# Performance work log

Hardware: AMD Instinct MI355X
Metric: run time of the kernel (lower is better)

The kernel has to match this reference:

```python
import jax, jax.numpy as jnp
import numpy as np

B, S, D, H = 2, 2048, 1024, 16
HD = D // H  # 64


def setup_inputs() -> dict:
    key = jax.random.key(0)
    ks = jax.random.split(key, 5)
    sc = 1.0 / np.sqrt(D)
    return {
        "x": jax.random.normal(ks[0], (B, S, D), jnp.float32),
        "wq": jax.random.normal(ks[1], (D, D), jnp.float32) * sc,
        "bq": jnp.zeros((D,), jnp.float32),
        "wk": jax.random.normal(ks[2], (D, D), jnp.float32) * sc,
        "bk": jnp.zeros((D,), jnp.float32),
        "wv": jax.random.normal(ks[3], (D, D), jnp.float32) * sc,
        "bv": jnp.zeros((D,), jnp.float32),
        "wo": jax.random.normal(ks[4], (D, D), jnp.float32) * sc,
        "bo": jnp.zeros((D,), jnp.float32),
    }


def _rope_tables(seq_len, dim):
    inv_freq = 1.0 / (10000.0 ** (jnp.arange(0, dim, 2, dtype=jnp.float32) / dim))
    t = jnp.arange(seq_len, dtype=jnp.float32)
    freqs = jnp.einsum("i,j->ij", t, inv_freq)  # [S, dim/2]
    emb = jnp.concatenate([freqs, freqs], axis=-1)  # [S, dim]
    return jnp.cos(emb)[None, None], jnp.sin(emb)[None, None]  # [1,1,S,dim]


def _rotate_half(x):
    x1, x2 = x[..., : x.shape[-1] // 2], x[..., x.shape[-1] // 2 :]
    return jnp.concatenate([-x2, x1], axis=-1)


def reference(x, wq, bq, wk, bk, wv, bv, wo, bo):
    b, s, d = x.shape
    h, hd = H, d // H
    # projections (torch Linear: x @ W.T + b) -> [b, h, s, hd]
    def proj(w, bias):
        return (x @ w.T + bias).reshape(b, s, h, hd).transpose(0, 2, 1, 3)

    q, k, v = proj(wq, bq), proj(wk, bk), proj(wv, bv)
    cos, sin = _rope_tables(s, hd)
    q = q * cos + _rotate_half(q) * sin
    k = k * cos + _rotate_half(k) * sin
    scores = jnp.einsum("bhqd,bhkd->bhqk", q, k) / jnp.sqrt(jnp.float32(hd))
    attn = jax.nn.softmax(scores, axis=-1)
    out = jnp.einsum("bhqk,bhkd->bhqd", attn, v)
    out = out.transpose(0, 2, 1, 3).reshape(b, s, d)
    return out @ wo.T + bo
```

## Files before the change

kernel.cpp:

```cpp
#include <hip/hip_runtime.h>
#include <hip/hip_bf16.h>

#define Bq 2
#define Sq 2048
#define Dq 1024
#define Hq 16
#define QSCALE 0.18033688011112042f

typedef __attribute__((ext_vector_type(8))) short short8;
typedef __attribute__((ext_vector_type(4))) float floatx4;
typedef unsigned short ushort_t;

#define VMCNT0() asm volatile("s_waitcnt vmcnt(0)" ::: "memory")
#define GLDS(src, dst) __builtin_amdgcn_global_load_lds( \
    (const __attribute__((address_space(1))) void*)(src), \
    (__attribute__((address_space(3))) void*)(dst), 16, 0, 0)

__device__ __forceinline__ ushort_t f2bf(float f) {
    union { float f; unsigned u; } v; v.f = f;
    unsigned u = v.u;
    u += 0x7fffu + ((u >> 16) & 1u);
    return (ushort_t)(u >> 16);
}

__device__ __forceinline__ unsigned pk_bf16(float a, float b) {
    union { __hip_bfloat162 h; unsigned u; } c;
    c.h = __float22bfloat162_rn(float2{a, b});
    return c.u;
}

__device__ __forceinline__ void cvt8(const float* __restrict__ in, ushort_t* __restrict__ out, int i) {
    const float4* p = (const float4*)in + (size_t)i * 2;
    float4 a = p[0], b = p[1];
    ushort4 lo, hi;
    lo.x = f2bf(a.x); lo.y = f2bf(a.y); lo.z = f2bf(a.z); lo.w = f2bf(a.w);
    hi.x = f2bf(b.x); hi.y = f2bf(b.y); hi.z = f2bf(b.z); hi.w = f2bf(b.w);
    *(ushort4*)(out + (size_t)i * 8)     = lo;
    *(ushort4*)(out + (size_t)i * 8 + 4) = hi;
}

__global__ void prep(const float* __restrict__ x,
                     const float* __restrict__ wq, const float* __restrict__ wk,
                     const float* __restrict__ wv, const float* __restrict__ wo,
                     ushort_t* __restrict__ xb,
                     ushort_t* __restrict__ wqb, ushort_t* __restrict__ wkb,
                     ushort_t* __restrict__ wvb, ushort_t* __restrict__ wob,
                     float* __restrict__ cost, float* __restrict__ sint) {
    int b = blockIdx.x;
    if (b < 2048) {
        cvt8(x, xb, b * 256 + threadIdx.x);
    } else if (b < 4096) {
        int w = (b - 2048) >> 9;
        int i = ((b - 2048) & 511) * 256 + threadIdx.x;
        const float* src = (w == 0) ? wq : (w == 1) ? wk : (w == 2) ? wv : wo;
        ushort_t* dst    = (w == 0) ? wqb : (w == 1) ? wkb : (w == 2) ? wvb : wob;
        cvt8(src, dst, i);
    } else {
        int i = (b - 4096) * 256 + threadIdx.x;
        int s = i >> 5, f = i & 31;
        float invf = powf(10000.0f, -(float)f / 32.0f);
        float ang = (float)s * invf;
        cost[i] = cosf(ang);
        sint[i] = sinf(ang);
    }
}

__global__ __launch_bounds__(256, 3) void gemm_qkv(
    const ushort_t* __restrict__ xb,
    const ushort_t* __restrict__ wqb, const ushort_t* __restrict__ wkb, const ushort_t* __restrict__ wvb,
    const float* __restrict__ bq, const float* __restrict__ bk, const float* __restrict__ bv,
    const float* __restrict__ cost, const float* __restrict__ sint,
    ushort_t* __restrict__ qout, ushort_t* __restrict__ kout, ushort_t* __restrict__ vtout)
{
    __shared__ ushort_t As0[128 * 32], As1[128 * 32];
    __shared__ ushort_t Bs0[128 * 32], Bs1[128 * 32];
    const int mode = blockIdx.z;
    const ushort_t* W  = (mode == 0) ? wqb : (mode == 1) ? wkb : wvb;
    const float* bias  = (mode == 0) ? bq  : (mode == 1) ? bk  : bv;

    const int t = threadIdx.x;
    const int lane = t & 63;
    const int wid = t >> 6;
    const int l15 = lane & 15, lk = lane >> 4;
    const int wr = wid >> 1, wc = wid & 1;
    const int rowBase = blockIdx.y * 128;
    const int colBase = blockIdx.x * 128;

    floatx4 acc[4][4] = {};

    const char* aSrc[2];
    const char* bSrc[2];
    int ldso[2];
#pragma unroll
    for (int issue = 0; issue < 2; ++issue) {
        int ldsoff = issue * 4096 + t * 16;
        int row = ldsoff >> 6;
        int cb  = ldsoff & 63;
        ldso[issue] = ldsoff;
        aSrc[issue] = (const char*)xb + (size_t)(rowBase + row) * 2048 + cb;
        bSrc[issue] = (const char*)W  + (size_t)(colBase + row) * 2048 + cb;
    }

    auto STAGE = [&](ushort_t* Ad, ushort_t* Bd) {
#pragma unroll
        for (int issue = 0; issue < 2; ++issue) {
            GLDS(aSrc[issue], (char*)Ad + ldso[issue]);
            GLDS(bSrc[issue], (char*)Bd + ldso[issue]);
        }
        aSrc[0] += 64; aSrc[1] += 64; bSrc[0] += 64; bSrc[1] += 64;
    };

    auto KSTEP = [&](const ushort_t* Ac, const ushort_t* Bc, int knext, ushort_t* An, ushort_t* Bn) {
        if (knext < Dq) STAGE(An, Bn);
        short8 a[4], b[4];
#pragma unroll
        for (int m = 0; m < 4; ++m)
            a[m] = *(const short8*)((const char*)Ac + (wr * 64 + m * 16 + l15) * 64 + lk * 16);
#pragma unroll
        for (int n = 0; n < 4; ++n)
            b[n] = *(const short8*)((const char*)Bc + (wc * 64 + n * 16 + l15) * 64 + lk * 16);
        __builtin_amdgcn_s_setprio(1);
#pragma unroll
        for (int m = 0; m < 4; ++m)
#pragma unroll
            for (int n = 0; n < 4; ++n)
                acc[m][n] = __builtin_amdgcn_mfma_f32_16x16x32_bf16(a[m], b[n], acc[m][n], 0, 0, 0);
        __builtin_amdgcn_s_setprio(0);
        VMCNT0();
        __syncthreads();
    };

    STAGE(As0, Bs0);
    VMCNT0();
    __syncthreads();

#pragma unroll 1
    for (int k0 = 0; k0 < Dq; k0 += 64) {
        KSTEP(As0, Bs0, k0 + 32, As1, Bs1);
        KSTEP(As1, Bs1, k0 + 64, As0, Bs0);
    }

    const int colW = colBase + wc * 64;
    const int hh = colW >> 6;

    if (mode < 2) {
        ushort_t* outp = (mode == 0) ? qout : kout;
        const float osc = (mode == 0) ? QSCALE : 1.0f;
#pragma unroll
        for (int m = 0; m < 4; ++m) {
            int rg0 = rowBase + wr * 64 + m * 16 + lk * 4;
#pragma unroll
            for (int n2 = 0; n2 < 2; ++n2) {
                int d0 = n2 * 16 + l15;
                float b0 = bias[colW + d0];
                float b2 = bias[colW + d0 + 32];
#pragma unroll
                for (int r = 0; r < 4; ++r) {
                    int rg = rg0 + r;
                    int bb = rg >> 11;
                    int s  = rg & 2047;
                    float c  = cost[s * 32 + d0];
                    float sn = sint[s * 32 + d0];
                    float a0 = acc[m][n2][r]     + b0;
                    float a2 = acc[m][n2 + 2][r] + b2;
                    float o0 = (a0 * c - a2 * sn) * osc;
                    float o2 = (a2 * c + a0 * sn) * osc;
                    size_t base = ((size_t)(bb * Hq + hh) * Sq + s) * 64;
                    outp[base + d0]      = f2bf(o0);
                    outp[base + d0 + 32] = f2bf(o2);
                }
            }
        }
    } else {
#pragma unroll
        for (int m = 0; m < 4; ++m) {
            int rg0 = rowBase + wr * 64 + m * 16 + lk * 4;
            int bb  = rg0 >> 11;
            int s0  = rg0 & 2047;
            int g   = (s0 & 63) >> 2;
            int ng  = (g >> 3) * 8 + (g & 3) * 2 + ((g >> 2) & 1);
            int s2b = (s0 & ~63) + ng * 4;
#pragma unroll
            for (int n = 0; n < 4; ++n) {
                int d = n * 16 + l15;
                float bb_ = bias[colW + d];
#pragma unroll
                for (int r = 0; r < 4; ++r)
                    vtout[((size_t)(bb * Hq + hh) * 64 + d) * Sq + s2b + r] = f2bf(acc[m][n][r] + bb_);
            }
        }
    }
}

__global__ __launch_bounds__(256, 3) void flash_attn(
    const ushort_t* __restrict__ qbuf, const ushort_t* __restrict__ kbuf,
    const ushort_t* __restrict__ vtbuf, ushort_t* __restrict__ abuf)
{
    __shared__ char Ks0[16384], Ks1[16384];
    __shared__ char Vs0[16384], Vs1[16384];

    const int t = threadIdx.x, lane = t & 63, wid = t >> 6;
    const int l15 = lane & 15, lk = lane >> 4;

    int flat = blockIdx.y * 16 + blockIdx.x;
    flat = (flat & 7) * 64 + (flat >> 3);
    const int qtile = flat & 15, bh = flat >> 4;
    const int bpos = bh >> 4, h = bh & 15;
    const int qbase = qtile * 128 + wid * 32;

    const ushort_t* Qp = qbuf + ((size_t)bh * Sq + qbase) * 64;
    short8 qf[2][2];
#pragma unroll
    for (int mq = 0; mq < 2; ++mq)
#pragma unroll
        for (int kk = 0; kk < 2; ++kk)
            qf[mq][kk] = *(const short8*)(Qp + (mq * 16 + l15) * 64 + kk * 32 + lk * 8);

    short8 onesf;
#pragma unroll
    for (int j = 0; j < 8; ++j) onesf[j] = (short)0x3F80;

    floatx4 oacc[2][4] = {};
    floatx4 lacc[2] = {};

    int off_[4][2];
#pragma unroll
    for (int n = 0; n < 4; ++n) {
        int swz = (l15 & 7) << 4;
#pragma unroll
        for (int kk = 0; kk < 2; ++kk)
            off_[n][kk] = (n * 16 + l15) * 128 + ((kk * 64 + lk * 16) ^ swz);
    }

    const char* Kg = (const char*)kbuf  + (size_t)bh * Sq * 128;
    const char* Vg = (const char*)vtbuf + (size_t)bh * 64 * Sq * 2;
    unsigned kOff[2], vOff[2];
    int ldso[2];
#pragma unroll
    for (int issue = 0; issue < 2; ++issue) {
        int ldsoff = issue * 4096 + t * 16;
        int row = ldsoff >> 7;
        int pb  = ldsoff & 127;
        int lb  = pb ^ ((row & 7) << 4);
        ldso[issue] = ldsoff;
        kOff[issue] = (unsigned)(row * 128 + lb);
        vOff[issue] = (unsigned)(row * 4096 + lb);
    }

    auto STAGE = [&](char* Kd, char* Vd) {
#pragma unroll
        for (int issue = 0; issue < 2; ++issue) {
            GLDS(Kg + kOff[issue],        Kd + ldso[issue]);
            GLDS(Kg + kOff[issue] + 8192, Kd + 8192 + ldso[issue]);
            GLDS(Vg + vOff[issue],        Vd + ldso[issue]);
            GLDS(Vg + vOff[issue] + 128,  Vd + 8192 + ldso[issue]);
        }
        kOff[0] += 16384; kOff[1] += 16384; vOff[0] += 256; vOff[1] += 256;
    };

    auto TILE = [&](const char* Kc, const char* Vc, bool doStage, char* Kn, char* Vn) {
        if (doStage) STAGE(Kn, Vn);

#pragma unroll
        for (int sub = 0; sub < 2; ++sub) {
            const char* Kcs = Kc + sub * 8192;
            const char* Vcs = Vc + sub * 8192;

            short8 kf[4][2];
#pragma unroll
            for (int n = 0; n < 4; ++n)
#pragma unroll
                for (int kk = 0; kk < 2; ++kk)
                    kf[n][kk] = *(const short8*)(Kcs + off_[n][kk]);

            floatx4 sacc[2][4] = {};
            __builtin_amdgcn_s_setprio(1);
#pragma unroll
            for (int kk = 0; kk < 2; ++kk)
#pragma unroll
                for (int n = 0; n < 4; ++n)
#pragma unroll
                    for (int mq = 0; mq < 2; ++mq)
                        sacc[mq][n] = __builtin_amdgcn_mfma_f32_16x16x32_bf16(kf[n][kk], qf[mq][kk], sacc[mq][n], 0, 0, 0);
            __builtin_amdgcn_s_setprio(0);

            short8 vf[4][2];
#pragma unroll
            for (int n = 0; n < 4; ++n)
#pragma unroll
                for (int kb = 0; kb < 2; ++kb)
                    vf[n][kb] = *(const short8*)(Vcs + off_[n][kb]);

            short8 paf[2][2];
#pragma unroll
            for (int mq = 0; mq < 2; ++mq) {
                float p[4][4];
#pragma unroll
                for (int n = 0; n < 4; ++n)
#pragma unroll
                    for (int r = 0; r < 4; ++r)
                        p[n][r] = __builtin_exp2f(sacc[mq][n][r]);
#pragma unroll
                for (int kb = 0; kb < 2; ++kb) {
                    union { unsigned u[4]; short8 v; } pu;
                    pu.u[0] = pk_bf16(p[2 * kb][0],     p[2 * kb][1]);
                    pu.u[1] = pk_bf16(p[2 * kb][2],     p[2 * kb][3]);
                    pu.u[2] = pk_bf16(p[2 * kb + 1][0], p[2 * kb + 1][1]);
                    pu.u[3] = pk_bf16(p[2 * kb + 1][2], p[2 * kb + 1][3]);
                    paf[mq][kb] = pu.v;
                }
            }

            __builtin_amdgcn_s_setprio(1);
#pragma unroll
            for (int kb = 0; kb < 2; ++kb) {
#pragma unroll
                for (int n = 0; n < 4; ++n)
#pragma unroll
                    for (int mq = 0; mq < 2; ++mq)
                        oacc[mq][n] = __builtin_amdgcn_mfma_f32_16x16x32_bf16(paf[mq][kb], vf[n][kb], oacc[mq][n], 0, 0, 0);
#pragma unroll
                for (int mq = 0; mq < 2; ++mq)
                    lacc[mq] = __builtin_amdgcn_mfma_f32_16x16x32_bf16(paf[mq][kb], onesf, lacc[mq], 0, 0, 0);
            }
            __builtin_amdgcn_s_setprio(0);
        }

        VMCNT0();
        __syncthreads();
    };

    STAGE(Ks0, Vs0);
    VMCNT0();
    __syncthreads();

#pragma unroll 1
    for (int i = 0; i < 7; ++i) {
        TILE(Ks0, Vs0, true, Ks1, Vs1);
        TILE(Ks1, Vs1, true, Ks0, Vs0);
    }
    TILE(Ks0, Vs0, true,  Ks1, Vs1);
    TILE(Ks1, Vs1, false, Ks0, Vs0);

#pragma unroll
    for (int mq = 0; mq < 2; ++mq)
#pragma unroll
        for (int r = 0; r < 4; ++r) {
            float linv = 1.0f / lacc[mq][r];
            int srow = qbase + mq * 16 + lk * 4 + r;
            size_t base = ((size_t)bpos * Sq + srow) * Dq + h * 64;
#pragma unroll
            for (int n = 0; n < 4; ++n)
                abuf[base + n * 16 + l15] = f2bf(oacc[mq][n][r] * linv);
        }
}

__global__ __launch_bounds__(256, 3) void gemm_out(
    const ushort_t* __restrict__ ab, const ushort_t* __restrict__ wob,
    const float* __restrict__ bo, float* __restrict__ out)
{
    __shared__ ushort_t As0[128 * 64], As1[128 * 64];
    __shared__ ushort_t Bs0[64 * 64],  Bs1[64 * 64];
    const int t = threadIdx.x;
    const int lane = t & 63;
    const int wid = t >> 6;
    const int l15 = lane & 15, lk = lane >> 4;
    const int wr = wid >> 1, wc = wid & 1;
    const int rowBase = blockIdx.y * 128;
    const int colBase = blockIdx.x * 64;

    floatx4 acc[4][2] = {};

    const int swz = (l15 & 7) << 4;
    int aoff_[4][2], boff_[2][2];
#pragma unroll
    for (int m = 0; m < 4; ++m)
#pragma unroll
        for (int kk = 0; kk < 2; ++kk)
            aoff_[m][kk] = (wr * 64 + m * 16 + l15) * 128 + ((kk * 64 + lk * 16) ^ swz);
#pragma unroll
    for (int n = 0; n < 2; ++n)
#pragma unroll
        for (int kk = 0; kk < 2; ++kk)
            boff_[n][kk] = (wc * 32 + n * 16 + l15) * 128 + ((kk * 64 + lk * 16) ^ swz);

    const char* aSrc[4];
    const char* bSrc[2];
    int ldsoA[4], ldsoB[2];
#pragma unroll
    for (int issue = 0; issue < 4; ++issue) {
        int ldsoff = issue * 4096 + t * 16;
        int row = ldsoff >> 7;
        int pb  = ldsoff & 127;
        int lb  = pb ^ ((row & 7) << 4);
        ldsoA[issue] = ldsoff;
        aSrc[issue] = (const char*)ab + (size_t)(rowBase + row) * 2048 + lb;
    }
#pragma unroll
    for (int issue = 0; issue < 2; ++issue) {
        int ldsoff = issue * 4096 + t * 16;
        int row = ldsoff >> 7;
        int pb  = ldsoff & 127;
        int lb  = pb ^ ((row & 7) << 4);
        ldsoB[issue] = ldsoff;
        bSrc[issue] = (const char*)wob + (size_t)(colBase + row) * 2048 + lb;
    }

    auto STAGE = [&](ushort_t* Ad, ushort_t* Bd) {
#pragma unroll
        for (int issue = 0; issue < 4; ++issue)
            GLDS(aSrc[issue], (char*)Ad + ldsoA[issue]);
#pragma unroll
        for (int issue = 0; issue < 2; ++issue)
            GLDS(bSrc[issue], (char*)Bd + ldsoB[issue]);
#pragma unroll
        for (int issue = 0; issue < 4; ++issue) aSrc[issue] += 128;
        bSrc[0] += 128; bSrc[1] += 128;
    };

    auto KSTEP = [&](const ushort_t* Ac, const ushort_t* Bc, int knext, ushort_t* An, ushort_t* Bn) {
        if (knext < Dq) STAGE(An, Bn);
        short8 a[4][2], b[2][2];
#pragma unroll
        for (int m = 0; m < 4; ++m)
#pragma unroll
            for (int kk = 0; kk < 2; ++kk)
                a[m][kk] = *(const short8*)((const char*)Ac + aoff_[m][kk]);
#pragma unroll
        for (int n = 0; n < 2; ++n)
#pragma unroll
            for (int kk = 0; kk < 2; ++kk)
                b[n][kk] = *(const short8*)((const char*)Bc + boff_[n][kk]);
        __builtin_amdgcn_s_setprio(1);
#pragma unroll
        for (int kk = 0; kk < 2; ++kk)
#pragma unroll
            for (int m = 0; m < 4; ++m)
#pragma unroll
                for (int n = 0; n < 2; ++n)
                    acc[m][n] = __builtin_amdgcn_mfma_f32_16x16x32_bf16(a[m][kk], b[n][kk], acc[m][n], 0, 0, 0);
        __builtin_amdgcn_s_setprio(0);
        VMCNT0();
        __syncthreads();
    };

    STAGE(As0, Bs0);
    VMCNT0();
    __syncthreads();

#pragma unroll 1
    for (int k0 = 0; k0 < Dq; k0 += 128) {
        KSTEP(As0, Bs0, k0 + 64,  As1, Bs1);
        KSTEP(As1, Bs1, k0 + 128, As0, Bs0);
    }

    const int colW = colBase + wc * 32;
#pragma unroll
    for (int m = 0; m < 4; ++m) {
        int rg0 = rowBase + wr * 64 + m * 16 + lk * 4;
#pragma unroll
        for (int n = 0; n < 2; ++n) {
            int colg = colW + n * 16 + l15;
            float bb_ = bo[colg];
#pragma unroll
            for (int r = 0; r < 4; ++r)
                out[(size_t)(rg0 + r) * Dq + colg] = acc[m][n][r] + bb_;
        }
    }
}

extern "C" void kernel_launch(void* const* d_in, const int* in_sizes, int n_in,
                              void* d_out, int out_size, void* d_ws, size_t ws_size,
                              hipStream_t stream) {
    (void)in_sizes; (void)n_in; (void)out_size;
    const float* x  = (const float*)d_in[0];
    const float* wq = (const float*)d_in[1];
    const float* bq = (const float*)d_in[2];
    const float* wk = (const float*)d_in[3];
    const float* bk = (const float*)d_in[4];
    const float* wv = (const float*)d_in[5];
    const float* bv = (const float*)d_in[6];
    const float* wo = (const float*)d_in[7];
    const float* bo = (const float*)d_in[8];
    float* out = (float*)d_out;

    if (ws_size < 50855936) return;
    char* ws = (char*)d_ws;
    ushort_t* xb   = (ushort_t*)(ws + 0);
    ushort_t* wqb  = (ushort_t*)(ws + 8388608);
    ushort_t* wkb  = (ushort_t*)(ws + 10485760);
    ushort_t* wvb  = (ushort_t*)(ws + 12582912);
    ushort_t* wob  = (ushort_t*)(ws + 14680064);
    ushort_t* qb   = (ushort_t*)(ws + 16777216);
    ushort_t* kb   = (ushort_t*)(ws + 25165824);
    ushort_t* vtb  = (ushort_t*)(ws + 33554432);
    ushort_t* abuf = (ushort_t*)(ws + 41943040);
    float*    cost = (float*)(ws + 50331648);
    float*    sint = (float*)(ws + 50593792);

    prep<<<4352, 256, 0, stream>>>(x, wq, wk, wv, wo, xb, wqb, wkb, wvb, wob, cost, sint);
    gemm_qkv<<<dim3(8, 32, 3), 256, 0, stream>>>(xb, wqb, wkb, wvb, bq, bk, bv, cost, sint, qb, kb, vtb);
    flash_attn<<<dim3(16, 32), 256, 0, stream>>>(qb, kb, vtb, abuf);
    gemm_out<<<dim3(16, 32), 256, 0, stream>>>(abuf, wob, bo, out);
}
```

Before: 119.4 us.

## Double QKV GEMM K-tile with swizzled LDS and halve attention KV tile

The QKV projection GEMM now stages 64-wide K slices (128-byte rows) instead of 32-wide ones. It uses an XOR swizzle on both the global source offsets and the LDS reads to avoid bank conflicts, and runs two MFMA k-substeps per barrier, halving the number of syncs. Launch bounds drop to 2 blocks per CU to fit the larger LDS footprint. Separately, the flash attention kernel shrinks its K/V tile from 128 to 64 keys per stage, doubling the loop count. This halves its LDS use, presumably for occupancy, at the cost of more barriers.

```diff
diff --git a/kernel.cpp b/kernel.cpp
--- a/kernel.cpp
+++ b/kernel.cpp
@@ -65,15 +65,15 @@
     }
 }
 
-__global__ __launch_bounds__(256, 3) void gemm_qkv(
+__global__ __launch_bounds__(256, 2) void gemm_qkv(
     const ushort_t* __restrict__ xb,
     const ushort_t* __restrict__ wqb, const ushort_t* __restrict__ wkb, const ushort_t* __restrict__ wvb,
     const float* __restrict__ bq, const float* __restrict__ bk, const float* __restrict__ bv,
     const float* __restrict__ cost, const float* __restrict__ sint,
     ushort_t* __restrict__ qout, ushort_t* __restrict__ kout, ushort_t* __restrict__ vtout)
 {
-    __shared__ ushort_t As0[128 * 32], As1[128 * 32];
-    __shared__ ushort_t Bs0[128 * 32], Bs1[128 * 32];
+    __shared__ ushort_t As0[128 * 64], As1[128 * 64];
+    __shared__ ushort_t Bs0[128 * 64], Bs1[128 * 64];
     const int mode = blockIdx.z;
     const ushort_t* W  = (mode == 0) ? wqb : (mode == 1) ? wkb : wvb;
     const float* bias  = (mode == 0) ? bq  : (mode == 1) ? bk  : bv;
@@ -88,43 +88,64 @@
 
     floatx4 acc[4][4] = {};
 
-    const char* aSrc[2];
-    const char* bSrc[2];
-    int ldso[2];
-#pragma unroll
-    for (int issue = 0; issue < 2; ++issue) {
+    const int swz = (l15 & 7) << 4;
+    int aoff_[4][2], boff_[4][2];
+#pragma unroll
+    for (int m = 0; m < 4; ++m)
+#pragma unroll
+        for (int kk = 0; kk < 2; ++kk)
+            aoff_[m][kk] = (wr * 64 + m * 16 + l15) * 128 + ((kk * 64 + lk * 16) ^ swz);
+#pragma unroll
+    for (int n = 0; n < 4; ++n)
+#pragma unroll
+        for (int kk = 0; kk < 2; ++kk)
+            boff_[n][kk] = (wc * 64 + n * 16 + l15) * 128 + ((kk * 64 + lk * 16) ^ swz);
+
+    const char* aSrc[4];
+    const char* bSrc[4];
+    int ldso[4];
+#pragma unroll
+    for (int issue = 0; issue < 4; ++issue) {
         int ldsoff = issue * 4096 + t * 16;
-        int row = ldsoff >> 6;
-        int cb  = ldsoff & 63;
+        int row = ldsoff >> 7;
+        int pb  = ldsoff & 127;
+        int lb  = pb ^ ((row & 7) << 4);
         ldso[issue] = ldsoff;
-        aSrc[issue] = (const char*)xb + (size_t)(rowBase + row) * 2048 + cb;
-        bSrc[issue] = (const char*)W  + (size_t)(colBase + row) * 2048 + cb;
+        aSrc[issue] = (const char*)xb + (size_t)(rowBase + row) * 2048 + lb;
+        bSrc[issue] = (const char*)W  + (size_t)(colBase + row) * 2048 + lb;
     }
 
     auto STAGE = [&](ushort_t* Ad, ushort_t* Bd) {
 #pragma unroll
-        for (int issue = 0; issue < 2; ++issue) {
+        for (int issue = 0; issue < 4; ++issue) {
             GLDS(aSrc[issue], (char*)Ad + ldso[issue]);
             GLDS(bSrc[issue], (char*)Bd + ldso[issue]);
         }
-        aSrc[0] += 64; aSrc[1] += 64; bSrc[0] += 64; bSrc[1] += 64;
+#pragma unroll
+        for (int issue = 0; issue < 4; ++issue) { aSrc[issue] += 128; bSrc[issue] += 128; }
     };
 
     auto KSTEP = [&](const ushort_t* Ac, const ushort_t* Bc, int knext, ushort_t* An, ushort_t* Bn) {
         if (knext < Dq) STAGE(An, Bn);
-        short8 a[4], b[4];
+        short8 a[4][2], b[4][2];
 #pragma unroll
         for (int m = 0; m < 4; ++m)
-            a[m] = *(const short8*)((const char*)Ac + (wr * 64 + m * 16 + l15) * 64 + lk * 16);
+#pragma unroll
+            for (int kk = 0; kk < 2; ++kk)
+                a[m][kk] = *(const short8*)((const char*)Ac + aoff_[m][kk]);
 #pragma unroll
         for (int n = 0; n < 4; ++n)
-            b[n] = *(const short8*)((const char*)Bc + (wc * 64 + n * 16 + l15) * 64 + lk * 16);
+#pragma unroll
+            for (int kk = 0; kk < 2; ++kk)
+                b[n][kk] = *(const short8*)((const char*)Bc + boff_[n][kk]);
         __builtin_amdgcn_s_setprio(1);
 #pragma unroll
-        for (int m = 0; m < 4; ++m)
-#pragma unroll
-            for (int n = 0; n < 4; ++n)
-                acc[m][n] = __builtin_amdgcn_mfma_f32_16x16x32_bf16(a[m], b[n], acc[m][n], 0, 0, 0);
+        for (int kk = 0; kk < 2; ++kk)
+#pragma unroll
+            for (int m = 0; m < 4; ++m)
+#pragma unroll
+                for (int n = 0; n < 4; ++n)
+                    acc[m][n] = __builtin_amdgcn_mfma_f32_16x16x32_bf16(a[m][kk], b[n][kk], acc[m][n], 0, 0, 0);
         __builtin_amdgcn_s_setprio(0);
         VMCNT0();
         __syncthreads();
@@ -135,9 +156,9 @@
     __syncthreads();
 
 #pragma unroll 1
-    for (int k0 = 0; k0 < Dq; k0 += 64) {
-        KSTEP(As0, Bs0, k0 + 32, As1, Bs1);
-        KSTEP(As1, Bs1, k0 + 64, As0, Bs0);
+    for (int k0 = 0; k0 < Dq; k0 += 128) {
+        KSTEP(As0, Bs0, k0 + 64,  As1, Bs1);
+        KSTEP(As1, Bs1, k0 + 128, As0, Bs0);
     }
 
     const int colW = colBase + wc * 64;
@@ -196,8 +217,8 @@
     const ushort_t* __restrict__ qbuf, const ushort_t* __restrict__ kbuf,
     const ushort_t* __restrict__ vtbuf, ushort_t* __restrict__ abuf)
 {
-    __shared__ char Ks0[16384], Ks1[16384];
-    __shared__ char Vs0[16384], Vs1[16384];
+    __shared__ char Ks0[64 * 128], Ks1[64 * 128];
+    __shared__ char Vs0[64 * 128], Vs1[64 * 128];
 
     const int t = threadIdx.x, lane = t & 63, wid = t >> 6;
     const int l15 = lane & 15, lk = lane >> 4;
@@ -250,81 +271,73 @@
     auto STAGE = [&](char* Kd, char* Vd) {
 #pragma unroll
         for (int issue = 0; issue < 2; ++issue) {
-            GLDS(Kg + kOff[issue],        Kd + ldso[issue]);
-            GLDS(Kg + kOff[issue] + 8192, Kd + 8192 + ldso[issue]);
-            GLDS(Vg + vOff[issue],        Vd + ldso[issue]);
-            GLDS(Vg + vOff[issue] + 128,  Vd + 8192 + ldso[issue]);
-        }
-        kOff[0] += 16384; kOff[1] += 16384; vOff[0] += 256; vOff[1] += 256;
+            GLDS(Kg + kOff[issue], Kd + ldso[issue]);
+            GLDS(Vg + vOff[issue], Vd + ldso[issue]);
+        }
+        kOff[0] += 8192; kOff[1] += 8192; vOff[0] += 128; vOff[1] += 128;
     };
 
     auto TILE = [&](const char* Kc, const char* Vc, bool doStage, char* Kn, char* Vn) {
         if (doStage) STAGE(Kn, Vn);
 
-#pragma unroll
-        for (int sub = 0; sub < 2; ++sub) {
-            const char* Kcs = Kc + sub * 8192;
-            const char* Vcs = Vc + sub * 8192;
-
-            short8 kf[4][2];
+        short8 kf[4][2];
+#pragma unroll
+        for (int n = 0; n < 4; ++n)
+#pragma unroll
+            for (int kk = 0; kk < 2; ++kk)
+                kf[n][kk] = *(const short8*)(Kc + off_[n][kk]);
+
+        floatx4 sacc[2][4] = {};
+        __builtin_amdgcn_s_setprio(1);
+#pragma unroll
+        for (int kk = 0; kk < 2; ++kk)
 #pragma unroll
             for (int n = 0; n < 4; ++n)
 #pragma unroll
-                for (int kk = 0; kk < 2; ++kk)
-                    kf[n][kk] = *(const short8*)(Kcs + off_[n][kk]);
-
-            floatx4 sacc[2][4] = {};
-            __builtin_amdgcn_s_setprio(1);
-#pragma unroll
-            for (int kk = 0; kk < 2; ++kk)
-#pragma unroll
-                for (int n = 0; n < 4; ++n)
-#pragma unroll
-                    for (int mq = 0; mq < 2; ++mq)
-                        sacc[mq][n] = __builtin_amdgcn_mfma_f32_16x16x32_bf16(kf[n][kk], qf[mq][kk], sacc[mq][n], 0, 0, 0);
-            __builtin_amdgcn_s_setprio(0);
-
-            short8 vf[4][2];
+                for (int mq = 0; mq < 2; ++mq)
+                    sacc[mq][n] = __builtin_amdgcn_mfma_f32_16x16x32_bf16(kf[n][kk], qf[mq][kk], sacc[mq][n], 0, 0, 0);
+        __builtin_amdgcn_s_setprio(0);
+
+        short8 vf[4][2];
+#pragma unroll
+        for (int n = 0; n < 4; ++n)
+#pragma unroll
+            for (int kb = 0; kb < 2; ++kb)
+                vf[n][kb] = *(const short8*)(Vc + off_[n][kb]);
+
+        short8 paf[2][2];
+#pragma unroll
+        for (int mq = 0; mq < 2; ++mq) {
+            float p[4][4];
 #pragma unroll
             for (int n = 0; n < 4; ++n)
 #pragma unroll
-                for (int kb = 0; kb < 2; ++kb)
-                    vf[n][kb] = *(const short8*)(Vcs + off_[n][kb]);
-
-            short8 paf[2][2];
-#pragma unroll
-            for (int mq = 0; mq < 2; ++mq) {
-                float p[4][4];
-#pragma unroll
-                for (int n = 0; n < 4; ++n)
-#pragma unroll
-                    for (int r = 0; r < 4; ++r)
-                        p[n][r] = __builtin_exp2f(sacc[mq][n][r]);
-#pragma unroll
-                for (int kb = 0; kb < 2; ++kb) {
-                    union { unsigned u[4]; short8 v; } pu;
-                    pu.u[0] = pk_bf16(p[2 * kb][0],     p[2 * kb][1]);
-                    pu.u[1] = pk_bf16(p[2 * kb][2],     p[2 * kb][3]);
-                    pu.u[2] = pk_bf16(p[2 * kb + 1][0], p[2 * kb + 1][1]);
-                    pu.u[3] = pk_bf16(p[2 * kb + 1][2], p[2 * kb + 1][3]);
-                    paf[mq][kb] = pu.v;
-                }
+                for (int r = 0; r < 4; ++r)
+                    p[n][r] = __builtin_exp2f(sacc[mq][n][r]);
+#pragma unroll
+            for (int kb = 0; kb < 2; ++kb) {
+                union { unsigned u[4]; short8 v; } pu;
+                pu.u[0] = pk_bf16(p[2 * kb][0],     p[2 * kb][1]);
+                pu.u[1] = pk_bf16(p[2 * kb][2],     p[2 * kb][3]);
+                pu.u[2] = pk_bf16(p[2 * kb + 1][0], p[2 * kb + 1][1]);
+                pu.u[3] = pk_bf16(p[2 * kb + 1][2], p[2 * kb + 1][3]);
+                paf[mq][kb] = pu.v;
             }
-
-            __builtin_amdgcn_s_setprio(1);
-#pragma unroll
-            for (int kb = 0; kb < 2; ++kb) {
-#pragma unroll
-                for (int n = 0; n < 4; ++n)
-#pragma unroll
-                    for (int mq = 0; mq < 2; ++mq)
-                        oacc[mq][n] = __builtin_amdgcn_mfma_f32_16x16x32_bf16(paf[mq][kb], vf[n][kb], oacc[mq][n], 0, 0, 0);
+        }
+
+        __builtin_amdgcn_s_setprio(1);
+#pragma unroll
+        for (int kb = 0; kb < 2; ++kb) {
+#pragma unroll
+            for (int n = 0; n < 4; ++n)
 #pragma unroll
                 for (int mq = 0; mq < 2; ++mq)
-                    lacc[mq] = __builtin_amdgcn_mfma_f32_16x16x32_bf16(paf[mq][kb], onesf, lacc[mq], 0, 0, 0);
-            }
-            __builtin_amdgcn_s_setprio(0);
-        }
+                    oacc[mq][n] = __builtin_amdgcn_mfma_f32_16x16x32_bf16(paf[mq][kb], vf[n][kb], oacc[mq][n], 0, 0, 0);
+#pragma unroll
+            for (int mq = 0; mq < 2; ++mq)
+                lacc[mq] = __builtin_amdgcn_mfma_f32_16x16x32_bf16(paf[mq][kb], onesf, lacc[mq], 0, 0, 0);
+        }
+        __builtin_amdgcn_s_setprio(0);
 
         VMCNT0();
         __syncthreads();
@@ -335,7 +348,7 @@
     __syncthreads();
 
 #pragma unroll 1
-    for (int i = 0; i < 7; ++i) {
+    for (int i = 0; i < 15; ++i) {
         TILE(Ks0, Vs0, true, Ks1, Vs1);
         TILE(Ks1, Vs1, true, Ks0, Vs0);
     }
```

Measured after the change: 119.3 us. Within noise of the previous version (-0.1%).
